# Performance work log

Hardware: AMD Instinct MI355X
Metric: run time of the kernel (lower is better)

Reference implementation:

```python
import jax, jax.numpy as jnp
import numpy as np

B, T, D = 4, 2048, 512
H, HS = 8, 64            # n_head, head_size
E, K = 8, 2              # num_experts, top_k
CAP = int(B * T * K / E * 1.0)  # expert capacity = 2048
EPS = 1e-5


def setup_inputs() -> dict:
    key = jax.random.key(0)
    ks = jax.random.split(key, 16)
    s = lambda k, shp, fan: jax.random.normal(k, shp, jnp.float32) * (fan ** -0.5)
    return {
        "x": jax.random.normal(ks[0], (B, T, D), jnp.float32),
        "ln1_g": jnp.ones((D,), jnp.float32), "ln1_b": jnp.zeros((D,), jnp.float32),
        "Wq": s(ks[1], (H, D, HS), D), "Wk": s(ks[2], (H, D, HS), D), "Wv": s(ks[3], (H, D, HS), D),
        "Wo": s(ks[4], (D, D), D), "bo": jnp.zeros((D,), jnp.float32),
        "ln2_g": jnp.ones((D,), jnp.float32), "ln2_b": jnp.zeros((D,), jnp.float32),
        "Wg": s(ks[5], (D, E), D), "bg": jnp.zeros((E,), jnp.float32),
        "Wn": s(ks[6], (D, E), D), "bn": jnp.zeros((E,), jnp.float32),
        "W1": s(ks[7], (E, D, 4 * D), D), "b1": jnp.zeros((E, 4 * D), jnp.float32),
        "W2": s(ks[8], (E, 4 * D, D), 4 * D), "b2": jnp.zeros((E, D), jnp.float32),
    }


def _ln(x, g, b):
    m = jnp.mean(x, -1, keepdims=True)
    v = jnp.var(x, -1, keepdims=True)
    return (x - m) * jax.lax.rsqrt(v + EPS) * g + b


def _attn(h, Wq, Wk, Wv, Wo, bo):
    q = jnp.einsum('btd,hde->bhte', h, Wq)
    k = jnp.einsum('btd,hde->bhte', h, Wk)
    v = jnp.einsum('btd,hde->bhte', h, Wv)
    # NOTE: source scales by C**-0.5 with C = n_embed (not head_size)
    wei = jnp.einsum('bhte,bhse->bhts', q, k) * (D ** -0.5)
    causal = jnp.tril(jnp.ones((T, T), bool))
    wei = jnp.where(causal, wei, -jnp.inf)
    wei = jax.nn.softmax(wei, axis=-1)
    out = jnp.einsum('bhts,bhse->bhte', wei, v)              # [B,H,T,HS]
    out = out.transpose(0, 2, 1, 3).reshape(B, T, D)          # concat heads
    return out @ Wo + bo


def _moe(h, Wg, bg, Wn, bn, W1, b1, W2, b2):
    logits = h @ Wg + bg
    noise_logits = h @ Wn + bn
    noise = jax.random.normal(jax.random.key(42), logits.shape, logits.dtype) * jax.nn.softplus(noise_logits)
    noisy = logits + noise
    vals, idx = jax.lax.top_k(noisy, K)                       # [B,T,K]
    # softmax over -inf-masked sparse logits == softmax over top-k values, scattered
    gates = (jax.nn.softmax(vals, -1)[..., None] * jax.nn.one_hot(idx, E, dtype=h.dtype)).sum(-2)  # [B,T,E]
    flat_x = h.reshape(-1, D)
    flat_g = gates.reshape(-1, E)
    flat_idx = idx.reshape(-1, K)
    N = flat_x.shape[0]
    mask = (flat_idx[None] == jnp.arange(E)[:, None, None]).any(-1)   # [E,N]
    rank = jnp.cumsum(mask, axis=1) - 1
    keep = mask & (rank < CAP)                                 # first CAP tokens per expert
    slot = jnp.where(keep, rank, CAP)
    tok = jnp.arange(N, dtype=jnp.int32)

    def build(s, kp):
        buf = jnp.zeros(CAP + 1, jnp.int32).at[s].set(tok)
        vb = jnp.zeros(CAP + 1, bool).at[s].set(kp)
        return buf[:CAP], vb[:CAP]

    idx_buf, valid = jax.vmap(build)(slot, keep)               # [E,CAP]
    xg = flat_x[idx_buf]                                       # [E,CAP,D]
    mid = jax.nn.relu(jnp.einsum('ecd,edf->ecf', xg, W1) + b1[:, None, :])
    out = jnp.einsum('ecf,efd->ecd', mid, W2) + b2[:, None, :]
    gate_sel = flat_g[idx_buf, jnp.arange(E)[:, None]]         # [E,CAP]
    w = out * (gate_sel * valid.astype(h.dtype))[..., None]
    upd = jnp.zeros_like(flat_x).at[idx_buf.reshape(-1)].add(w.reshape(-1, D))
    return upd.reshape(h.shape)


def reference(x, ln1_g, ln1_b, Wq, Wk, Wv, Wo, bo, ln2_g, ln2_b,
              Wg, bg, Wn, bn, W1, b1, W2, b2):
    x = x + _attn(_ln(x, ln1_g, ln1_b), Wq, Wk, Wv, Wo, bo)
    x = x + _moe(_ln(x, ln2_g, ln2_b), Wg, bg, Wn, bn, W1, b1, W2, b2)
    return x
```

## Files before the change

kernel.cpp:

```cpp
#include <hip/hip_runtime.h>
#include <math.h>

#define TSEQ 2048
#define DD   512
#define NH   8
#define HSZ  64
#define NE   8
#define NTOK 8192
#define CAPK 2048
#define FF   2048

typedef __bf16 bf16x8 __attribute__((ext_vector_type(8)));
typedef float  f32x4  __attribute__((ext_vector_type(4)));
typedef unsigned int u32;
typedef u32 u32x2 __attribute__((ext_vector_type(2)));
typedef short s16x4 __attribute__((ext_vector_type(4)));

#define WAITVM(N) asm volatile("s_waitcnt vmcnt(" #N ")" ::: "memory")

__device__ __forceinline__ void gload16(const void* g, void* l){
  __builtin_amdgcn_global_load_lds((const __attribute__((address_space(1))) u32*)g,
                                   (__attribute__((address_space(3))) u32*)l, 16, 0, 0);
}

__device__ __forceinline__ u32 pkbf(float a, float b){
  unsigned short ua = __builtin_bit_cast(unsigned short, (__bf16)a);
  unsigned short ub = __builtin_bit_cast(unsigned short, (__bf16)b);
  return (u32)ua | ((u32)ub << 16);
}

__device__ __forceinline__ u32 pksplit(float v){
  __bf16 hb = (__bf16)v;
  __bf16 lb = (__bf16)(v - (float)hb);
  return (u32)__builtin_bit_cast(unsigned short, hb) |
         ((u32)__builtin_bit_cast(unsigned short, lb) << 16);
}

__device__ __forceinline__ s16x4 mk4(u32 a, u32 b){
  u32x2 t; t[0] = a; t[1] = b;
  return __builtin_bit_cast(s16x4, t);
}

__device__ __forceinline__ unsigned rotl32(unsigned x, int r){ return (x<<r)|(x>>(32-r)); }

__device__ __forceinline__ void threefry2x32(unsigned c0, unsigned c1, unsigned &o0, unsigned &o1){
  const unsigned k0 = 0u, k1 = 42u;
  const unsigned k2 = k0 ^ k1 ^ 0x1BD11BDAu;
  unsigned x0 = c0 + k0, x1 = c1 + k1;
#define TFR(rot) { x0 += x1; x1 = rotl32(x1, rot); x1 ^= x0; }
  TFR(13) TFR(15) TFR(26) TFR(6)   x0 += k1; x1 += k2 + 1u;
  TFR(17) TFR(29) TFR(16) TFR(24)  x0 += k2; x1 += k0 + 2u;
  TFR(13) TFR(15) TFR(26) TFR(6)   x0 += k0; x1 += k1 + 3u;
  TFR(17) TFR(29) TFR(16) TFR(24)  x0 += k1; x1 += k2 + 4u;
  TFR(13) TFR(15) TFR(26) TFR(6)   x0 += k2; x1 += k0 + 5u;
#undef TFR
  o0 = x0; o1 = x1;
}

__device__ __forceinline__ float erfinv_f(float x){
  float w = -log1pf(-x*x);
  float p;
  if (w < 5.0f){
    w -= 2.5f;
    p = 2.81022636e-08f;
    p = fmaf(p,w, 3.43273939e-07f);
    p = fmaf(p,w,-3.5233877e-06f);
    p = fmaf(p,w,-4.39150654e-06f);
    p = fmaf(p,w, 0.00021858087f);
    p = fmaf(p,w,-0.00125372503f);
    p = fmaf(p,w,-0.00417768164f);
    p = fmaf(p,w, 0.246640727f);
    p = fmaf(p,w, 1.50140941f);
  } else {
    w = sqrtf(w) - 3.0f;
    p = -0.000200214257f;
    p = fmaf(p,w, 0.000100950558f);
    p = fmaf(p,w, 0.00134934322f);
    p = fmaf(p,w,-0.00367342844f);
    p = fmaf(p,w, 0.00573950773f);
    p = fmaf(p,w,-0.0076224613f);
    p = fmaf(p,w, 0.00943887047f);
    p = fmaf(p,w, 1.00167406f);
    p = fmaf(p,w, 2.83297682f);
  }
  return p * x;
}

__global__ __launch_bounds__(256) void prep_kernel(
    const float* __restrict__ x, const float* __restrict__ ln1g, const float* __restrict__ ln1b,
    __bf16* __restrict__ h1hi, __bf16* __restrict__ h1lo,
    const float* __restrict__ Wq, const float* __restrict__ Wk, const float* __restrict__ Wv,
    __bf16* __restrict__ Bqh, __bf16* __restrict__ Bql,
    const float* __restrict__ Wo, __bf16* __restrict__ WoTh, __bf16* __restrict__ WoTl)
{
  __shared__ float t[64][65];
  int blk = blockIdx.x;
  int tid = threadIdx.x;
  if (blk < 2048){
    int row  = blk*4 + (tid >> 6);
    int lane = tid & 63;
    const float* xr = x + (size_t)row*DD;
    float4 a = *(const float4*)(xr + lane*4);
    float4 c = *(const float4*)(xr + 256 + lane*4);
    float s  = a.x+a.y+a.z+a.w + c.x+c.y+c.z+c.w;
    float ss = a.x*a.x+a.y*a.y+a.z*a.z+a.w*a.w + c.x*c.x+c.y*c.y+c.z*c.z+c.w*c.w;
    #pragma unroll
    for (int off = 32; off; off >>= 1){ s += __shfl_xor(s, off); ss += __shfl_xor(ss, off); }
    float m   = s * (1.0f/DD);
    float var = ss * (1.0f/DD) - m*m;
    float r   = 1.0f / sqrtf(var + 1e-5f);
    float4 g1 = *(const float4*)(ln1g + lane*4);
    float4 b1 = *(const float4*)(ln1b + lane*4);
    float4 g2 = *(const float4*)(ln1g + 256 + lane*4);
    float4 b2 = *(const float4*)(ln1b + 256 + lane*4);
    float f1[4], f2[4];
    f1[0]=(a.x-m)*r*g1.x+b1.x; f1[1]=(a.y-m)*r*g1.y+b1.y; f1[2]=(a.z-m)*r*g1.z+b1.z; f1[3]=(a.w-m)*r*g1.w+b1.w;
    f2[0]=(c.x-m)*r*g2.x+b2.x; f2[1]=(c.y-m)*r*g2.y+b2.y; f2[2]=(c.z-m)*r*g2.z+b2.z; f2[3]=(c.w-m)*r*g2.w+b2.w;
    __bf16 h1v[4] __attribute__((aligned(8))), l1v[4] __attribute__((aligned(8)));
    __bf16 h2v[4] __attribute__((aligned(8))), l2v[4] __attribute__((aligned(8)));
    #pragma unroll
    for (int j = 0; j < 4; ++j){
      __bf16 hb = (__bf16)f1[j]; h1v[j]=hb; l1v[j]=(__bf16)(f1[j]-(float)hb);
      __bf16 hc = (__bf16)f2[j]; h2v[j]=hc; l2v[j]=(__bf16)(f2[j]-(float)hc);
    }
    size_t base = (size_t)row*DD + lane*4;
    *(uint2*)(h1hi + base)       = *(const uint2*)h1v;
    *(uint2*)(h1lo + base)       = *(const uint2*)l1v;
    *(uint2*)(h1hi + base + 256) = *(const uint2*)h2v;
    *(uint2*)(h1lo + base + 256) = *(const uint2*)l2v;
  } else if (blk < 2240){
    int bx = blk - 2048;
    int kt = (bx & 7) * 64;
    int z  = bx >> 3;
    int sel = z >> 3, hh = z & 7;
    const float* W = (sel==0 ? Wq : (sel==1 ? Wk : Wv)) + (size_t)hh*DD*HSZ;
    int r = tid>>2, c0 = (tid&3)*16;
    #pragma unroll
    for (int j = 0; j < 16; j += 4){
      float4 v = *(const float4*)&W[(size_t)(kt+r)*HSZ + c0 + j];
      t[r][c0+j]=v.x; t[r][c0+j+1]=v.y; t[r][c0+j+2]=v.z; t[r][c0+j+3]=v.w;
    }
    __syncthreads();
    __bf16 hb[16] __attribute__((aligned(32)));
    __bf16 lb[16] __attribute__((aligned(32)));
    #pragma unroll
    for (int j = 0; j < 16; ++j){
      float f = t[c0+j][r];
      __bf16 h = (__bf16)f; hb[j]=h; lb[j]=(__bf16)(f-(float)h);
    }
    size_t off = (size_t)(z*64 + r)*512 + kt + c0;
    *(uint4*)(Bqh+off) = ((const uint4*)hb)[0]; *(uint4*)(Bqh+off+8) = ((const uint4*)hb)[1];
    *(uint4*)(Bql+off) = ((const uint4*)lb)[0]; *(uint4*)(Bql+off+8) = ((const uint4*)lb)[1];
  } else {
    int bx = blk - 2240;
    int nt = (bx & 7) * 64, mt = (bx >> 3) * 64;
    int r = tid>>2, c0 = (tid&3)*16;
    #pragma unroll
    for (int j = 0; j < 16; j += 4){
      float4 v = *(const float4*)&Wo[(size_t)(mt+r)*DD + nt + c0 + j];
      t[r][c0+j]=v.x; t[r][c0+j+1]=v.y; t[r][c0+j+2]=v.z; t[r][c0+j+3]=v.w;
    }
    __syncthreads();
    __bf16 hb[16] __attribute__((aligned(32)));
    __bf16 lb[16] __attribute__((aligned(32)));
    #pragma unroll
    for (int j = 0; j < 16; ++j){
      float f = t[c0+j][r];
      __bf16 h = (__bf16)f; hb[j]=h; lb[j]=(__bf16)(f-(float)h);
    }
    size_t off = (size_t)(nt + r)*DD + mt + c0;
    *(uint4*)(WoTh+off) = ((const uint4*)hb)[0]; *(uint4*)(WoTh+off+8) = ((const uint4*)hb)[1];
    *(uint4*)(WoTl+off) = ((const uint4*)lb)[0]; *(uint4*)(WoTl+off+8) = ((const uint4*)lb)[1];
  }
}

template<int MODE, int NN>
__global__ __launch_bounds__(256) void gemm_mfma3(
    const __bf16* __restrict__ Ahi, const __bf16* __restrict__ Alo,
    const __bf16* __restrict__ Bhi, const __bf16* __restrict__ Blo,
    const float* __restrict__ bias, const float* __restrict__ res, float* __restrict__ C,
    __bf16* __restrict__ qh, __bf16* __restrict__ ql,
    __bf16* __restrict__ kh, __bf16* __restrict__ kl,
    __bf16* __restrict__ vth, __bf16* __restrict__ vtl,
    int M, int N, int K)
{
  __shared__ __align__(16) char smem[65536];
  __bf16* AsH = (__bf16*)smem;
  __bf16* AsL = (__bf16*)(smem + 16384);
  __bf16* BsH = (__bf16*)(smem + 32768);
  __bf16* BsL = (__bf16*)(smem + 49152);

  int flat  = blockIdx.x;
  int chunk = flat / (8*NN);
  int rem   = flat % (8*NN);
  int mloc  = rem & 7;
  int nn    = rem >> 3;
  int m0 = (chunk*8 + mloc)*128;
  int n0 = nn*128;

  int tid = threadIdx.x;
  int w = tid>>6, l = tid&63;
  int wm = w>>1, wn = w&1;
  int srow = w*32 + (l>>2);
  int skb  = (l&3)<<4;
  const char* agh = (const char*)(Ahi + (size_t)(m0+srow)*K) + skb;
  const char* agl = (const char*)(Alo + (size_t)(m0+srow)*K) + skb;
  const char* bgh = (const char*)(Bhi + (size_t)(n0+srow)*K) + skb;
  const char* bgl = (const char*)(Blo + (size_t)(n0+srow)*K) + skb;
  size_t r16 = (size_t)16*K*sizeof(__bf16);

  f32x4 acc[4][4] = {};
  int rl = l & 15, kh_ = l >> 4;
  const __bf16* abh = AsH + (wm*64 + rl)*32 + kh_*8;
  const __bf16* abl = AsL + (wm*64 + rl)*32 + kh_*8;
  const __bf16* bbh = BsH + (wn*64 + rl)*32 + kh_*8;
  const __bf16* bbl = BsL + (wn*64 + rl)*32 + kh_*8;

  auto STAGE = [&](int bb, int kt){
    size_t o = (size_t)kt*64;
    gload16(agh+o,     AsH + bb*4096 + w*1024);
    gload16(agh+o+r16, AsH + bb*4096 + w*1024+512);
    gload16(agl+o,     AsL + bb*4096 + w*1024);
    gload16(agl+o+r16, AsL + bb*4096 + w*1024+512);
    gload16(bgh+o,     BsH + bb*4096 + w*1024);
    gload16(bgh+o+r16, BsH + bb*4096 + w*1024+512);
    gload16(bgl+o,     BsL + bb*4096 + w*1024);
    gload16(bgl+o+r16, BsL + bb*4096 + w*1024+512);
  };

  int nkt = K >> 5;
  STAGE(0, 0);
  for (int kt = 0; kt < nkt; ++kt){
    int bb = kt & 1;
    if (kt + 1 < nkt){ STAGE(bb^1, kt+1); WAITVM(8); }
    else             { WAITVM(0); }
    __builtin_amdgcn_s_barrier();
    bf16x8 afh[4], afl[4], bfh[4], bfl[4];
    #pragma unroll
    for (int i = 0; i < 4; ++i){
      afh[i] = *(const bf16x8*)(abh + bb*4096 + i*512);
      afl[i] = *(const bf16x8*)(abl + bb*4096 + i*512);
      bfh[i] = *(const bf16x8*)(bbh + bb*4096 + i*512);
      bfl[i] = *(const bf16x8*)(bbl + bb*4096 + i*512);
    }
    #pragma unroll
    for (int fm = 0; fm < 4; ++fm)
      #pragma unroll
      for (int fn = 0; fn < 4; ++fn){
        acc[fm][fn] = __builtin_amdgcn_mfma_f32_16x16x32_bf16(afh[fm], bfl[fn], acc[fm][fn], 0, 0, 0);
        acc[fm][fn] = __builtin_amdgcn_mfma_f32_16x16x32_bf16(afl[fm], bfh[fn], acc[fm][fn], 0, 0, 0);
        acc[fm][fn] = __builtin_amdgcn_mfma_f32_16x16x32_bf16(afh[fm], bfh[fn], acc[fm][fn], 0, 0, 0);
      }
    __builtin_amdgcn_s_barrier();
  }

  int ccol = l & 15, cr = (l >> 4) * 4;
  if (MODE == 0){
    #pragma unroll
    for (int fn = 0; fn < 4; ++fn){
      int n = n0 + wn*64 + fn*16 + ccol;
      float bv = bias[n];
      #pragma unroll
      for (int fm = 0; fm < 4; ++fm){
        int mb = m0 + wm*64 + fm*16 + cr;
        #pragma unroll
        for (int r = 0; r < 4; ++r){
          float v = acc[fm][fn][r] + bv + res[(size_t)(mb+r)*N + n];
          C[(size_t)(mb+r)*N + n] = v;
        }
      }
    }
  } else {
    u32 (*eps)[132] = (u32(*)[132])smem;
    int sel = n0 >> 9;
    int b   = m0 >> 11;
    int tb  = m0 & 2047;
    int dbase = n0 & 511;
    const float qsc = 0.04419417382415922f * 1.4426950408889634f;
    float sc = (sel == 0) ? qsc : 1.0f;
    #pragma unroll
    for (int p = 0; p < 2; ++p){
      __syncthreads();
      if (sel < 2){
        if (wm == p){
          #pragma unroll
          for (int fm = 0; fm < 4; ++fm)
            #pragma unroll
            for (int fn = 0; fn < 4; ++fn)
              #pragma unroll
              for (int r = 0; r < 4; ++r)
                eps[fm*16 + cr + r][wn*64 + fn*16 + ccol] = pksplit(acc[fm][fn][r] * sc);
        }
        __syncthreads();
        int row = tid >> 2, q4 = tid & 3;
        int hh = (dbase >> 6) + (q4 >> 1);
        int e0 = (q4 & 1) * 32;
        const u32* src = &eps[row][q4*32];
        __bf16 hbuf[32] __attribute__((aligned(16)));
        __bf16 lbuf[32] __attribute__((aligned(16)));
        #pragma unroll
        for (int j = 0; j < 32; ++j){
          u32 pk = src[j];
          hbuf[j] = __builtin_bit_cast(__bf16, (unsigned short)(pk & 0xffffu));
          lbuf[j] = __builtin_bit_cast(__bf16, (unsigned short)(pk >> 16));
        }
        size_t off = ((size_t)(b*8 + hh)*TSEQ + tb + p*64 + row)*64 + e0;
        __bf16* dh = sel ? kh : qh;
        __bf16* dl = sel ? kl : ql;
        #pragma unroll
        for (int j = 0; j < 4; ++j){
          *(uint4*)(dh + off + j*8) = ((const uint4*)hbuf)[j];
          *(uint4*)(dl + off + j*8) = ((const uint4*)lbuf)[j];
        }
      } else {
        if (wn == p){
          #pragma unroll
          for (int fn = 0; fn < 4; ++fn)
            #pragma unroll
            for (int fm = 0; fm < 4; ++fm){
              u32 pk4[4] __attribute__((aligned(16)));
              #pragma unroll
              for (int r = 0; r < 4; ++r)
                pk4[r] = pksplit(acc[fm][fn][r]);
              *(uint4*)&eps[fn*16 + ccol][wm*64 + fm*16 + cr] = *(const uint4*)pk4;
            }
        }
        __syncthreads();
        int col = tid >> 2, tq = tid & 3;
        int d = dbase + p*64 + col;
        int hh = d >> 6, e = d & 63;
        const u32* src = &eps[col][tq*32];
        __bf16 hbuf[32] __attribute__((aligned(16)));
        __bf16 lbuf[32] __attribute__((aligned(16)));
        #pragma unroll
        for (int j = 0; j < 32; ++j){
          u32 pk = src[j];
          hbuf[j] = __builtin_bit_cast(__bf16, (unsigned short)(pk & 0xffffu));
          lbuf[j] = __builtin_bit_cast(__bf16, (unsigned short)(pk >> 16));
        }
        size_t off = ((size_t)(b*8 + hh)*64 + e)*TSEQ + tb + tq*32;
        #pragma unroll
        for (int j = 0; j < 4; ++j){
          *(uint4*)(vth + off + j*8) = ((const uint4*)hbuf)[j];
          *(uint4*)(vtl + off + j*8) = ((const uint4*)lbuf)[j];
        }
      }
    }
  }
}

template<int STORE_BF16, int RELU, int GATHER, int LOGN, int EBITS>
__global__ __launch_bounds__(256) void gemm_mfma(
    const __bf16* __restrict__ A, const __bf16* __restrict__ Bt,
    const float* __restrict__ bias, void* __restrict__ Cv,
    const int* __restrict__ idxb, int M, int N, int K)
{
  __shared__ __bf16 Asl[2][4096];
  __shared__ __bf16 Bsl[2][4096];
  int flat = blockIdx.x;
  int e = flat & ((1<<EBITS)-1);
  int tile = flat >> EBITS;
  int n0 = (tile & ((1<<LOGN)-1)) * 128;
  int m0 = (tile >> LOGN) * 128;
  const __bf16* Be = Bt + (size_t)e*N*K;
  const float*  be = bias + (size_t)e*N;
  int tid = threadIdx.x;
  int w = tid>>6, l = tid&63;
  int wm = w>>1, wn = w&1;
  int srow = w*32 + (l>>2);
  int skb  = (l&3)<<4;
  const char* ag;
  if (GATHER){
    int tok = idxb[e*CAPK + m0 + srow];
    ag = (const char*)(A + (size_t)tok*K) + skb;
  } else {
    ag = (const char*)(A + (size_t)e*M*K + (size_t)(m0 + srow)*K) + skb;
  }
  const char* bg = (const char*)(Be + (size_t)(n0 + srow)*K) + skb;
  size_t r16;
  if (GATHER){
    int tok2 = idxb[e*CAPK + m0 + srow + 16];
    r16 = (size_t)((const char*)(A + (size_t)tok2*K) + skb - ag);
  } else {
    r16 = (size_t)16*K*sizeof(__bf16);
  }

  f32x4 acc[4][4] = {};
  int rl = l & 15, kh = l >> 4;
  const __bf16* abase = &Asl[0][(wm*64 + rl)*32 + kh*8];
  const __bf16* bbase = &Bsl[0][(wn*64 + rl)*32 + kh*8];

  size_t br16 = (size_t)16*K*sizeof(__bf16);
  auto STAGE = [&](int bb, int kt){
    size_t o = (size_t)kt*64;
    gload16(ag+o,      &Asl[bb][w*1024]);
    gload16(ag+o+r16,  &Asl[bb][w*1024+512]);
    gload16(bg+o,      &Bsl[bb][w*1024]);
    gload16(bg+o+br16, &Bsl[bb][w*1024+512]);
  };

  int nkt = K >> 5;
  STAGE(0, 0);
  for (int kt = 0; kt < nkt; ++kt){
    int bb = kt & 1;
    if (kt + 1 < nkt){ STAGE(bb^1, kt+1); WAITVM(4); }
    else             { WAITVM(0); }
    __builtin_amdgcn_s_barrier();
    bf16x8 af[4], bf[4];
    #pragma unroll
    for (int i = 0; i < 4; ++i){
      af[i] = *(const bf16x8*)(abase + bb*4096 + i*512);
      bf[i] = *(const bf16x8*)(bbase + bb*4096 + i*512);
    }
    #pragma unroll
    for (int fm = 0; fm < 4; ++fm)
      #pragma unroll
      for (int fn = 0; fn < 4; ++fn)
        acc[fm][fn] = __builtin_amdgcn_mfma_f32_16x16x32_bf16(af[fm], bf[fn], acc[fm][fn], 0, 0, 0);
    __builtin_amdgcn_s_barrier();
  }

  int ccol = l & 15, cr = (l >> 4) * 4;
  char* Ce = (char*)Cv + (size_t)e*M*N*(STORE_BF16 ? 2 : 4);
  #pragma unroll
  for (int fn = 0; fn < 4; ++fn){
    int n = n0 + wn*64 + fn*16 + ccol;
    float bv = be[n];
    #pragma unroll
    for (int fm = 0; fm < 4; ++fm){
      int mb = m0 + wm*64 + fm*16 + cr;
      #pragma unroll
      for (int r = 0; r < 4; ++r){
        float v = acc[fm][fn][r] + bv;
        if (RELU) v = fmaxf(v, 0.f);
        if (STORE_BF16) ((__bf16*)Ce)[(size_t)(mb+r)*N + n] = (__bf16)v;
        else            ((float*)Ce)[(size_t)(mb+r)*N + n] = v;
      }
    }
  }
}

__global__ __launch_bounds__(256) void transp_conv2(const float* __restrict__ W1,
    const float* __restrict__ W2, __bf16* __restrict__ d1, __bf16* __restrict__ d2)
{
  __shared__ __bf16 t[64][72];
  int e = blockIdx.z;
  int id = blockIdx.x;
  const float* s; __bf16* d; int Ms, Ns, mt, nt;
  if (id < 256){ s = W1; d = d1; Ms = DD; Ns = FF; nt = (id&31)*64; mt = (id>>5)*64; }
  else { int i2 = id-256; s = W2; d = d2; Ms = FF; Ns = DD; nt = (i2&7)*64; mt = (i2>>3)*64; }
  s += (size_t)e*Ms*Ns;
  d += (size_t)e*Ms*Ns;
  int tid = threadIdx.x;
  int r = tid>>2, c0 = (tid&3)*16;
  #pragma unroll
  for (int j = 0; j < 16; j += 4){
    float4 v = *(const float4*)&s[(size_t)(mt+r)*Ns + nt + c0 + j];
    t[r][c0+j]   = (__bf16)v.x; t[r][c0+j+1] = (__bf16)v.y;
    t[r][c0+j+2] = (__bf16)v.z; t[r][c0+j+3] = (__bf16)v.w;
  }
  __syncthreads();
  __bf16 tmp[16] __attribute__((aligned(32)));
  #pragma unroll
  for (int j = 0; j < 16; ++j) tmp[j] = t[c0+j][r];
  uint4* dp = (uint4*)&d[(size_t)(nt+r)*Ms + mt + c0];
  dp[0] = ((const uint4*)tmp)[0];
  dp[1] = ((const uint4*)tmp)[1];
}

__global__ __launch_bounds__(512) void attn_mfma(
    const __bf16* __restrict__ qhi_g, const __bf16* __restrict__ qlo_g,
    const __bf16* __restrict__ khi_g, const __bf16* __restrict__ klo_g,
    const __bf16* __restrict__ vthi_g, const __bf16* __restrict__ vtlo_g,
    __bf16* __restrict__ ahi, __bf16* __restrict__ alo)
{
  extern __shared__ __align__(16) char ldsbuf[];
  int bh = blockIdx.x;
  int qtA = blockIdx.y, qtB = 15 - qtA;
  int b = bh >> 3, h = bh & 7;
  int tid = threadIdx.x;
  int w = tid >> 6, l = tid & 63;
  int g = l >> 4, r = l & 15;

  int qb[2]; qb[0] = qtA*128 + w*16; qb[1] = qtB*128 + (7-w)*16;
  int kdiag[2]; kdiag[0] = qtA; kdiag[1] = qtB;

  bf16x8 qhi[2][2], qlo[2][2];
  #pragma unroll
  for (int qf = 0; qf < 2; ++qf)
    #pragma unroll
    for (int ks = 0; ks < 2; ++ks){
      size_t qoff = ((size_t)bh*TSEQ + qb[qf] + r)*64 + ks*32 + g*8;
      qhi[qf][ks] = *(const bf16x8*)(qhi_g + qoff);
      qlo[qf][ks] = *(const bf16x8*)(qlo_g + qoff);
    }

  f32x4 ot[4][2] = {};
  float m_r[2] = {-INFINITY, -INFINITY};
  float l_r[2] = {0.f, 0.f};

  int nkt = qtB + 1;
  size_t kbase = (size_t)bh*TSEQ*64;
  size_t vbase = (size_t)bh*64*TSEQ;

  auto STAGE = [&](int buf, int kt){
    int row = tid >> 3, cc = tid & 7;
    char* base = ldsbuf + buf*65536 + (w << 10);
    #pragma unroll
    for (int p = 0; p < 2; ++p){
      int krow = p*64 + row;
      int ksw = (cc ^ (krow & 7)) * 8;
      gload16(khi_g + kbase + (size_t)(kt*128 + krow)*64 + ksw, base + p*8192);
      gload16(klo_g + kbase + (size_t)(kt*128 + krow)*64 + ksw, base + 16384 + p*8192);
      int vch = p*8 + cc;
      int vsw = ((vch ^ (row & 7)) & 15) * 8;
      gload16(vthi_g + vbase + (size_t)row*TSEQ + kt*128 + vsw, base + 32768 + p*8192);
      gload16(vtlo_g + vbase + (size_t)row*TSEQ + kt*128 + vsw, base + 49152 + p*8192);
    }
  };

  STAGE(0, 0);

  for (int kt = 0; kt < nkt; ++kt){
    int buf = kt & 1;
    if (kt + 1 < nkt){ STAGE(buf ^ 1, kt + 1); WAITVM(8); }
    else             { WAITVM(0); }
    __builtin_amdgcn_s_barrier();

    bool act[2];
    act[0] = (kt <= kdiag[0]);
    act[1] = true;

    const char* K0 = ldsbuf + buf*65536;
    const char* K1 = K0 + 16384;
    const char* V0 = K0 + 32768;
    const char* V1 = K0 + 49152;

    f32x4 s[8][2] = {};
    #pragma unroll
    for (int kf = 0; kf < 8; ++kf){
      int rowk = kf*16 + r;
      int rsw = (rowk & 7) << 4;
      #pragma unroll
      for (int ks = 0; ks < 2; ++ks){
        int off = rowk*128 + ((((ks*4 + g) << 4)) ^ rsw);
        bf16x8 khf = *(const bf16x8*)(K0 + off);
        bf16x8 klf = *(const bf16x8*)(K1 + off);
        #pragma unroll
        for (int qf = 0; qf < 2; ++qf){
          if (act[qf]){
            s[kf][qf] = __builtin_amdgcn_mfma_f32_16x16x32_bf16(khf, qlo[qf][ks], s[kf][qf], 0,0,0);
            s[kf][qf] = __builtin_amdgcn_mfma_f32_16x16x32_bf16(klf, qhi[qf][ks], s[kf][qf], 0,0,0);
            s[kf][qf] = __builtin_amdgcn_mfma_f32_16x16x32_bf16(khf, qhi[qf][ks], s[kf][qf], 0,0,0);
          }
        }
      }
    }

    #pragma unroll
    for (int qf = 0; qf < 2; ++qf){
      if (act[qf]){
        int q = qb[qf] + r;
        float mx = -INFINITY;
        if (kt == kdiag[qf]){
          #pragma unroll
          for (int kf = 0; kf < 8; ++kf)
            #pragma unroll
            for (int e = 0; e < 4; ++e){
              int key = kt*128 + kf*16 + g*4 + e;
              float sv = (key <= q) ? s[kf][qf][e] : -INFINITY;
              s[kf][qf][e] = sv;
              mx = fmaxf(mx, sv);
            }
        } else {
          #pragma unroll
          for (int kf = 0; kf < 8; ++kf)
            #pragma unroll
            for (int e = 0; e < 4; ++e)
              mx = fmaxf(mx, s[kf][qf][e]);
        }
        mx = fmaxf(mx, __shfl_xor(mx, 16));
        mx = fmaxf(mx, __shfl_xor(mx, 32));
        if (__any(mx > m_r[qf])){
          float mn = fmaxf(m_r[qf], mx);
          float fj = exp2f(m_r[qf] - mn);
          m_r[qf] = mn;
          l_r[qf] *= fj;
          #pragma unroll
          for (int ef = 0; ef < 4; ++ef)
            #pragma unroll
            for (int e = 0; e < 4; ++e)
              ot[ef][qf][e] *= fj;
        }
        float ts = 0.f;
        #pragma unroll
        for (int kf = 0; kf < 8; ++kf)
          #pragma unroll
          for (int e = 0; e < 4; ++e){
            float pv = exp2f(s[kf][qf][e] - m_r[qf]);
            s[kf][qf][e] = pv; ts += pv;
          }
        ts += __shfl_xor(ts, 16); ts += __shfl_xor(ts, 32);
        l_r[qf] += ts;
      }
    }

    #pragma unroll
    for (int kf = 0; kf < 8; ++kf){
      u32 PH[2][2], PL[2][2];
      #pragma unroll
      for (int qf = 0; qf < 2; ++qf){
        if (act[qf]){
          float p0 = s[kf][qf][0], p1 = s[kf][qf][1], p2 = s[kf][qf][2], p3 = s[kf][qf][3];
          __bf16 h0=(__bf16)p0, h1=(__bf16)p1, h2=(__bf16)p2, h3=(__bf16)p3;
          PH[qf][0] = pkbf(p0, p1);
          PH[qf][1] = pkbf(p2, p3);
          PL[qf][0] = pkbf(p0-(float)h0, p1-(float)h1);
          PL[qf][1] = pkbf(p2-(float)h2, p3-(float)h3);
        }
      }
      int chunk = 2*kf + (g>>1);
      int pb = (chunk >> 3) << 13;
      int cl = chunk & 7;
      #pragma unroll
      for (int ef = 0; ef < 4; ++ef){
        int rowv = ef*16 + r;
        int off = pb + rowv*128 + ((cl ^ (rowv & 7)) << 4) + (g&1)*8;
        s16x4 vh = *(const s16x4*)(V0 + off);
        s16x4 vl = *(const s16x4*)(V1 + off);
        #pragma unroll
        for (int qf = 0; qf < 2; ++qf){
          if (act[qf]){
            s16x4 ph = mk4(PH[qf][0], PH[qf][1]);
            s16x4 pl = mk4(PL[qf][0], PL[qf][1]);
            ot[ef][qf] = __builtin_amdgcn_mfma_f32_16x16x16bf16_1k(vh, pl, ot[ef][qf], 0,0,0);
            ot[ef][qf] = __builtin_amdgcn_mfma_f32_16x16x16bf16_1k(vl, ph, ot[ef][qf], 0,0,0);
            ot[ef][qf] = __builtin_amdgcn_mfma_f32_16x16x16bf16_1k(vh, ph, ot[ef][qf], 0,0,0);
          }
        }
      }
    }
    __builtin_amdgcn_s_barrier();
  }

  float* Osh = (float*)ldsbuf;
  #pragma unroll
  for (int qf = 0; qf < 2; ++qf){
    float inv = 1.0f / l_r[qf];
    int qloc = (qf ? (7-w) : w)*16 + r;
    #pragma unroll
    for (int ef = 0; ef < 4; ++ef)
      #pragma unroll
      for (int e = 0; e < 4; ++e)
        Osh[qloc*68 + ef*16 + g*4 + e] = ot[ef][qf][e] * inv;
    __syncthreads();
    {
      int qt = qf ? qtB : qtA;
      int q = tid >> 2, e0 = (tid & 3)*16;
      const float* srow = Osh + q*68 + e0;
      size_t base = ((size_t)(b*TSEQ + qt*128 + q))*DD + h*64 + e0;
      #pragma unroll
      for (int j = 0; j < 4; ++j){
        float4 v = *(const float4*)(srow + j*4);
        float f[4] = {v.x, v.y, v.z, v.w};
        __bf16 hb[4] __attribute__((aligned(8)));
        __bf16 lb[4] __attribute__((aligned(8)));
        #pragma unroll
        for (int q2 = 0; q2 < 4; ++q2){
          __bf16 h2b = (__bf16)f[q2];
          hb[q2] = h2b; lb[q2] = (__bf16)(f[q2] - (float)h2b);
        }
        *(uint2*)(ahi + base + j*4) = *(const uint2*)hb;
        *(uint2*)(alo + base + j*4) = *(const uint2*)lb;
      }
    }
    __syncthreads();
  }
}

__global__ __launch_bounds__(256) void routerln_kernel(const float* __restrict__ x1,
    const float* __restrict__ gw, const float* __restrict__ bw,
    const float* __restrict__ Wg, const float* __restrict__ bg,
    const float* __restrict__ Wn, const float* __restrict__ bn,
    __bf16* __restrict__ h2b,
    int* __restrict__ idx0, int* __restrict__ idx1,
    float* __restrict__ g0, float* __restrict__ g1)
{
  int wid = threadIdx.x >> 6, lane = threadIdx.x & 63;
  int tok = blockIdx.x*4 + wid;
  const float* xr = x1 + (size_t)tok*DD;
  float4 a = *(const float4*)(xr + lane*4);
  float4 c = *(const float4*)(xr + 256 + lane*4);
  float s  = a.x+a.y+a.z+a.w + c.x+c.y+c.z+c.w;
  float ss = a.x*a.x+a.y*a.y+a.z*a.z+a.w*a.w + c.x*c.x+c.y*c.y+c.z*c.z+c.w*c.w;
  #pragma unroll
  for (int off = 32; off; off >>= 1){ s += __shfl_xor(s, off); ss += __shfl_xor(ss, off); }
  float m   = s * (1.0f/DD);
  float var = ss * (1.0f/DD) - m*m;
  float rr  = 1.0f / sqrtf(var + 1e-5f);
  float4 g1v = *(const float4*)(gw + lane*4);
  float4 b1v = *(const float4*)(bw + lane*4);
  float4 g2v = *(const float4*)(gw + 256 + lane*4);
  float4 b2v = *(const float4*)(bw + 256 + lane*4);
  float f1[4], f2[4];
  f1[0]=(a.x-m)*rr*g1v.x+b1v.x; f1[1]=(a.y-m)*rr*g1v.y+b1v.y; f1[2]=(a.z-m)*rr*g1v.z+b1v.z; f1[3]=(a.w-m)*rr*g1v.w+b1v.w;
  f2[0]=(c.x-m)*rr*g2v.x+b2v.x; f2[1]=(c.y-m)*rr*g2v.y+b2v.y; f2[2]=(c.z-m)*rr*g2v.z+b2v.z; f2[3]=(c.w-m)*rr*g2v.w+b2v.w;
  {
    __bf16 h1v[4] __attribute__((aligned(8)));
    __bf16 h2v[4] __attribute__((aligned(8)));
    #pragma unroll
    for (int j = 0; j < 4; ++j){ h1v[j] = (__bf16)f1[j]; h2v[j] = (__bf16)f2[j]; }
    size_t base = (size_t)tok*DD + lane*4;
    *(uint2*)(h2b + base)       = *(const uint2*)h1v;
    *(uint2*)(h2b + base + 256) = *(const uint2*)h2v;
  }
  float ag[8] = {0,0,0,0,0,0,0,0}, an[8] = {0,0,0,0,0,0,0,0};
  int d1 = lane*4, d2 = 256 + lane*4;
  #pragma unroll
  for (int j = 0; j < 4; ++j){
    const float* wg1 = Wg + (size_t)(d1+j)*8;
    const float* wn1 = Wn + (size_t)(d1+j)*8;
    const float* wg2 = Wg + (size_t)(d2+j)*8;
    const float* wn2 = Wn + (size_t)(d2+j)*8;
    #pragma unroll
    for (int e = 0; e < 8; ++e){
      ag[e] = fmaf(f1[j], wg1[e], ag[e]); an[e] = fmaf(f1[j], wn1[e], an[e]);
      ag[e] = fmaf(f2[j], wg2[e], ag[e]); an[e] = fmaf(f2[j], wn2[e], an[e]);
    }
  }
  #pragma unroll
  for (int off = 32; off; off >>= 1){
    #pragma unroll
    for (int e = 0; e < 8; ++e){ ag[e] += __shfl_xor(ag[e], off); an[e] += __shfl_xor(an[e], off); }
  }
  __shared__ float ns[4][8];
  if (lane < 8){
    int e = lane;
    float lg = ag[e] + bg[e];
    float nl = an[e] + bn[e];
    float sp = fmaxf(nl, 0.f) + log1pf(expf(-fabsf(nl)));
    unsigned i = (unsigned)(tok*8 + e);
    unsigned r0b, r1b;
    threefry2x32(0u, i, r0b, r1b);
    unsigned bits = r0b ^ r1b;
    float f = __uint_as_float((bits >> 9) | 0x3f800000u) - 1.0f;
    float u = fmaf(f, 2.0f, -0.99999994f);
    u = fmaxf(u, -0.99999994f);
    float z = 1.41421356f * erfinv_f(u);
    ns[wid][e] = lg + z*sp;
  }
  __syncthreads();
  if (lane == 0){
    float v0 = -INFINITY; int i0 = 0;
    #pragma unroll
    for (int e = 0; e < 8; ++e){ float v = ns[wid][e]; if (v > v0){ v0 = v; i0 = e; } }
    float v1 = -INFINITY; int i1 = 0;
    #pragma unroll
    for (int e = 0; e < 8; ++e){ if (e != i0){ float v = ns[wid][e]; if (v > v1){ v1 = v; i1 = e; } } }
    float dexp = expf(v1 - v0);
    float ssum = 1.0f + dexp;
    idx0[tok] = i0; idx1[tok] = i1;
    g0[tok] = 1.0f/ssum; g1[tok] = dexp/ssum;
  }
}

__global__ __launch_bounds__(256) void route_scan(const int* __restrict__ idx0,
    const int* __restrict__ idx1, int* __restrict__ idx_buf, int* __restrict__ tok_slot)
{
  int e = blockIdx.x, tid = threadIdx.x;
  for (int i = tid; i < CAPK; i += 256) idx_buf[e*CAPK + i] = 0;
  __syncthreads();
  int base = tid * 32;
  int cnt = 0;
  for (int j = 0; j < 32; ++j){ int t = base + j; cnt += (idx0[t]==e || idx1[t]==e) ? 1 : 0; }
  __shared__ int ps[256];
  ps[tid] = cnt; __syncthreads();
  for (int off = 1; off < 256; off <<= 1){
    int add = (tid >= off) ? ps[tid - off] : 0;
    __syncthreads();
    ps[tid] += add;
    __syncthreads();
  }
  int slot = ps[tid] - cnt;
  for (int j = 0; j < 32; ++j){
    int t = base + j;
    int k = (idx0[t]==e) ? 0 : ((idx1[t]==e) ? 1 : -1);
    if (k >= 0){
      if (slot < CAPK){ idx_buf[e*CAPK + slot] = t; tok_slot[t*2 + k] = slot; }
      else            { tok_slot[t*2 + k] = -1; }
      slot++;
    }
  }
}

__global__ __launch_bounds__(128) void combine_kernel(const float* __restrict__ x1,
    const __bf16* __restrict__ eout, const int* __restrict__ idx0, const int* __restrict__ idx1,
    const float* __restrict__ g0, const float* __restrict__ g1,
    const int* __restrict__ tok_slot, float* __restrict__ outp)
{
  int n = blockIdx.x, t = threadIdx.x;
  float4 acc = *(const float4*)(x1 + (size_t)n*DD + t*4);
  #pragma unroll
  for (int k = 0; k < 2; ++k){
    int s = tok_slot[n*2 + k];
    if (s >= 0){
      int e  = (k==0) ? idx0[n] : idx1[n];
      float g = (k==0) ? g0[n] : g1[n];
      __bf16 vb[4] __attribute__((aligned(8)));
      *(uint2*)vb = *(const uint2*)(eout + ((size_t)(e*CAPK + s))*DD + t*4);
      acc.x = fmaf(g, (float)vb[0], acc.x); acc.y = fmaf(g, (float)vb[1], acc.y);
      acc.z = fmaf(g, (float)vb[2], acc.z); acc.w = fmaf(g, (float)vb[3], acc.w);
    }
  }
  *(float4*)(outp + (size_t)n*DD + t*4) = acc;
}

extern "C" void kernel_launch(void* const* d_in, const int* in_sizes, int n_in,
                              void* d_out, int out_size, void* d_ws, size_t ws_size,
                              hipStream_t stream)
{
  const float* x    = (const float*)d_in[0];
  const float* ln1g = (const float*)d_in[1];
  const float* ln1b = (const float*)d_in[2];
  const float* Wq   = (const float*)d_in[3];
  const float* Wk   = (const float*)d_in[4];
  const float* Wv   = (const float*)d_in[5];
  const float* Wo   = (const float*)d_in[6];
  const float* bo   = (const float*)d_in[7];
  const float* ln2g = (const float*)d_in[8];
  const float* ln2b = (const float*)d_in[9];
  const float* Wg   = (const float*)d_in[10];
  const float* bg   = (const float*)d_in[11];
  const float* Wn   = (const float*)d_in[12];
  const float* bn   = (const float*)d_in[13];
  const float* W1   = (const float*)d_in[14];
  const float* b1   = (const float*)d_in[15];
  const float* W2   = (const float*)d_in[16];
  const float* b2   = (const float*)d_in[17];
  float* out = (float*)d_out;
  char* ws = (char*)d_ws;
  const size_t MB = 1u << 20;

  (void)hipFuncSetAttribute((const void*)attn_mfma,
      hipFuncAttributeMaxDynamicSharedMemorySize, 131072);

  __bf16* h1hi   = (__bf16*)(ws);
  __bf16* h1lo   = (__bf16*)(ws + 8*MB);
  __bf16* attnhi = (__bf16*)(ws);
  __bf16* attnlo = (__bf16*)(ws + 8*MB);
  __bf16* h2b    = (__bf16*)(ws);
  __bf16* Qhi    = (__bf16*)(ws + 16*MB);
  __bf16* Qlo    = (__bf16*)(ws + 24*MB);
  __bf16* Khi    = (__bf16*)(ws + 32*MB);
  __bf16* Klo    = (__bf16*)(ws + 40*MB);
  __bf16* Vthi   = (__bf16*)(ws + 48*MB);
  __bf16* Vtlo   = (__bf16*)(ws + 56*MB);
  __bf16* W1T    = (__bf16*)(ws + 16*MB);
  __bf16* W2T    = (__bf16*)(ws + 32*MB);
  __bf16* eoutb  = (__bf16*)(ws + 48*MB);
  float*  x1     = (float*)(ws + 64*MB);
  __bf16* Bqh    = (__bf16*)(ws + 80*MB);
  __bf16* Bql    = (__bf16*)(ws + 82*MB);
  __bf16* mid    = (__bf16*)(ws + 80*MB);
  __bf16* WoTh   = (__bf16*)(ws + 144*MB);
  __bf16* WoTl   = (__bf16*)(ws + 144*MB + 512*1024);
  char*   smallp = ws + 145*MB;
  int*   idx0     = (int*)smallp;
  int*   idx1     = idx0 + NTOK;
  float* g0       = (float*)(idx1 + NTOK);
  float* g1       = g0 + NTOK;
  int*   tok_slot = (int*)(g1 + NTOK);
  int*   idx_buf  = tok_slot + NTOK*2;

  prep_kernel<<<dim3(2304), 256, 0, stream>>>(x, ln1g, ln1b, h1hi, h1lo,
      Wq, Wk, Wv, Bqh, Bql, Wo, WoTh, WoTl);
  gemm_mfma3<1,12><<<dim3(64*12), 256, 0, stream>>>(h1hi, h1lo, Bqh, Bql,
      nullptr, nullptr, nullptr, Qhi, Qlo, Khi, Klo, Vthi, Vtlo, NTOK, 1536, DD);
  attn_mfma<<<dim3(32, 8), 512, 131072, stream>>>(Qhi, Qlo, Khi, Klo, Vthi, Vtlo, attnhi, attnlo);
  gemm_mfma3<0,4><<<dim3(64*4), 256, 0, stream>>>(attnhi, attnlo, WoTh, WoTl,
      bo, x, x1, nullptr, nullptr, nullptr, nullptr, nullptr, nullptr, NTOK, DD, DD);
  routerln_kernel<<<dim3(NTOK/4), 256, 0, stream>>>(x1, ln2g, ln2b, Wg, bg, Wn, bn,
      h2b, idx0, idx1, g0, g1);
  transp_conv2<<<dim3(512,1,NE), 256, 0, stream>>>(W1, W2, W1T, W2T);
  route_scan<<<dim3(NE), 256, 0, stream>>>(idx0, idx1, idx_buf, tok_slot);
  gemm_mfma<1,1,1,4,3><<<dim3(8*16*16), 256, 0, stream>>>(
      h2b, W1T, b1, mid, idx_buf, CAPK, FF, DD);
  gemm_mfma<1,0,0,2,3><<<dim3(8*16*4), 256, 0, stream>>>(
      mid, W2T, b2, eoutb, nullptr, CAPK, DD, FF);
  combine_kernel<<<dim3(NTOK), 128, 0, stream>>>(x1, eoutb, idx0, idx1, g0, g1, tok_slot, out);
}
```

Before: 362.9 us.

## Triple-buffer expert GEMM, merge route scan into weight transpose, lazy softmax rescale

```diff
diff --git a/kernel.cpp b/kernel.cpp
--- a/kernel.cpp
+++ b/kernel.cpp
@@ -355,8 +355,8 @@
     const float* __restrict__ bias, void* __restrict__ Cv,
     const int* __restrict__ idxb, int M, int N, int K)
 {
-  __shared__ __bf16 Asl[2][4096];
-  __shared__ __bf16 Bsl[2][4096];
+  __shared__ __bf16 Asl[3][4096];
+  __shared__ __bf16 Bsl[3][4096];
   int flat = blockIdx.x;
   int e = flat & ((1<<EBITS)-1);
   int tile = flat >> EBITS;
@@ -401,10 +401,12 @@
 
   int nkt = K >> 5;
   STAGE(0, 0);
+  STAGE(1, 1);
+  int bb = 0, st = 2;
   for (int kt = 0; kt < nkt; ++kt){
-    int bb = kt & 1;
-    if (kt + 1 < nkt){ STAGE(bb^1, kt+1); WAITVM(4); }
-    else             { WAITVM(0); }
+    if (kt + 2 < nkt){ STAGE(st, kt+2); WAITVM(8); }
+    else if (kt + 1 < nkt){ WAITVM(4); }
+    else { WAITVM(0); }
     __builtin_amdgcn_s_barrier();
     bf16x8 af[4], bf[4];
     #pragma unroll
@@ -418,6 +420,8 @@
       for (int fn = 0; fn < 4; ++fn)
         acc[fm][fn] = __builtin_amdgcn_mfma_f32_16x16x32_bf16(af[fm], bf[fn], acc[fm][fn], 0, 0, 0);
     __builtin_amdgcn_s_barrier();
+    bb = (bb == 2) ? 0 : bb + 1;
+    st = (st == 2) ? 0 : st + 1;
   }
 
   int ccol = l & 15, cr = (l >> 4) * 4;
@@ -440,18 +444,46 @@
   }
 }
 
-__global__ __launch_bounds__(256) void transp_conv2(const float* __restrict__ W1,
-    const float* __restrict__ W2, __bf16* __restrict__ d1, __bf16* __restrict__ d2)
+__global__ __launch_bounds__(256) void transp_scan(const float* __restrict__ W1,
+    const float* __restrict__ W2, __bf16* __restrict__ d1, __bf16* __restrict__ d2,
+    const int* __restrict__ idx0, const int* __restrict__ idx1,
+    int* __restrict__ idx_buf, int* __restrict__ tok_slot)
 {
   __shared__ __bf16 t[64][72];
+  __shared__ int ps[256];
   int e = blockIdx.z;
   int id = blockIdx.x;
+  int tid = threadIdx.x;
+  if (id == 512){
+    for (int i = tid; i < CAPK; i += 256) idx_buf[e*CAPK + i] = 0;
+    __syncthreads();
+    int base = tid * 32;
+    int cnt = 0;
+    for (int j = 0; j < 32; ++j){ int tt = base + j; cnt += (idx0[tt]==e || idx1[tt]==e) ? 1 : 0; }
+    ps[tid] = cnt; __syncthreads();
+    for (int off = 1; off < 256; off <<= 1){
+      int add = (tid >= off) ? ps[tid - off] : 0;
+      __syncthreads();
+      ps[tid] += add;
+      __syncthreads();
+    }
+    int slot = ps[tid] - cnt;
+    for (int j = 0; j < 32; ++j){
+      int tt = base + j;
+      int k = (idx0[tt]==e) ? 0 : ((idx1[tt]==e) ? 1 : -1);
+      if (k >= 0){
+        if (slot < CAPK){ idx_buf[e*CAPK + slot] = tt; tok_slot[tt*2 + k] = slot; }
+        else            { tok_slot[tt*2 + k] = -1; }
+        slot++;
+      }
+    }
+    return;
+  }
   const float* s; __bf16* d; int Ms, Ns, mt, nt;
   if (id < 256){ s = W1; d = d1; Ms = DD; Ns = FF; nt = (id&31)*64; mt = (id>>5)*64; }
   else { int i2 = id-256; s = W2; d = d2; Ms = FF; Ns = DD; nt = (i2&7)*64; mt = (i2>>3)*64; }
   s += (size_t)e*Ms*Ns;
   d += (size_t)e*Ms*Ns;
-  int tid = threadIdx.x;
   int r = tid>>2, c0 = (tid&3)*16;
   #pragma unroll
   for (int j = 0; j < 16; j += 4){
@@ -581,7 +613,7 @@
         }
         mx = fmaxf(mx, __shfl_xor(mx, 16));
         mx = fmaxf(mx, __shfl_xor(mx, 32));
-        if (__any(mx > m_r[qf])){
+        if (__any(mx > m_r[qf] + 8.0f)){
           float mn = fmaxf(m_r[qf], mx);
           float fj = exp2f(m_r[qf] - mn);
           m_r[qf] = mn;
@@ -764,35 +796,6 @@
   }
 }
 
-__global__ __launch_bounds__(256) void route_scan(const int* __restrict__ idx0,
-    const int* __restrict__ idx1, int* __restrict__ idx_buf, int* __restrict__ tok_slot)
-{
-  int e = blockIdx.x, tid = threadIdx.x;
-  for (int i = tid; i < CAPK; i += 256) idx_buf[e*CAPK + i] = 0;
-  __syncthreads();
-  int base = tid * 32;
-  int cnt = 0;
-  for (int j = 0; j < 32; ++j){ int t = base + j; cnt += (idx0[t]==e || idx1[t]==e) ? 1 : 0; }
-  __shared__ int ps[256];
-  ps[tid] = cnt; __syncthreads();
-  for (int off = 1; off < 256; off <<= 1){
-    int add = (tid >= off) ? ps[tid - off] : 0;
-    __syncthreads();
-    ps[tid] += add;
-    __syncthreads();
-  }
-  int slot = ps[tid] - cnt;
-  for (int j = 0; j < 32; ++j){
-    int t = base + j;
-    int k = (idx0[t]==e) ? 0 : ((idx1[t]==e) ? 1 : -1);
-    if (k >= 0){
-      if (slot < CAPK){ idx_buf[e*CAPK + slot] = t; tok_slot[t*2 + k] = slot; }
-      else            { tok_slot[t*2 + k] = -1; }
-      slot++;
-    }
-  }
-}
-
 __global__ __launch_bounds__(128) void combine_kernel(const float* __restrict__ x1,
     const __bf16* __restrict__ eout, const int* __restrict__ idx0, const int* __restrict__ idx1,
     const float* __restrict__ g0, const float* __restrict__ g1,
@@ -881,8 +884,8 @@
       bo, x, x1, nullptr, nullptr, nullptr, nullptr, nullptr, nullptr, NTOK, DD, DD);
   routerln_kernel<<<dim3(NTOK/4), 256, 0, stream>>>(x1, ln2g, ln2b, Wg, bg, Wn, bn,
       h2b, idx0, idx1, g0, g1);
-  transp_conv2<<<dim3(512,1,NE), 256, 0, stream>>>(W1, W2, W1T, W2T);
-  route_scan<<<dim3(NE), 256, 0, stream>>>(idx0, idx1, idx_buf, tok_slot);
+  transp_scan<<<dim3(513,1,NE), 256, 0, stream>>>(W1, W2, W1T, W2T,
+      idx0, idx1, idx_buf, tok_slot);
   gemm_mfma<1,1,1,4,3><<<dim3(8*16*16), 256, 0, stream>>>(
       h2b, W1T, b1, mid, idx_buf, CAPK, FF, DD);
   gemm_mfma<1,0,0,2,3><<<dim3(8*16*4), 256, 0, stream>>>(
```

After: 355.6 us. -2.0%, faster.
